# Optimization experiments

Measured on AMD Instinct MI355X. Metric: run time of the kernel, lower is better.

The kernel has to match this reference:

```python
import jax, jax.numpy as jnp
import numpy as np

S, B, E, H, AW = 4096, 2, 768, 12, 512  # seq, batch, embed, heads, attention_window


def _longformer_local_attn(query, Wq, bq, Wk, bk, Wv, bv):
    # query: [S, B, E] (seq-first, as in the torch module); returns [S, B, E]
    S_, B_, E_ = query.shape
    H_ = H
    D = E_ // H_
    W = AW // 2  # one-sided window (HF Longformer uses window//2 each side)
    x = query.transpose(1, 0, 2)  # [B, S, E]

    q = (x @ Wq + bq).reshape(B_, S_, H_, D) * (1.0 / jnp.sqrt(jnp.asarray(D, x.dtype)))
    k = (x @ Wk + bk).reshape(B_, S_, H_, D)
    v = (x @ Wv + bv).reshape(B_, S_, H_, D)

    nc = S_ // W  # number of query chunks of size W
    # pad keys/values by W on each side so every chunk sees a 3W key window
    kp = jnp.pad(k, ((0, 0), (W, W), (0, 0), (0, 0)))
    vp = jnp.pad(v, ((0, 0), (W, W), (0, 0), (0, 0)))
    # padded-coordinate indices of the 3W key window for each chunk: [nc, 3W]
    idx = jnp.arange(nc)[:, None] * W + jnp.arange(3 * W)[None, :]
    kc = kp[:, idx]  # [B, nc, 3W, H, D]
    vc = vp[:, idx]  # [B, nc, 3W, H, D]
    qc = q.reshape(B_, nc, W, H_, D)

    # banded scores: [B, H, nc, W, 3W]
    scores = jnp.einsum('bcqhd,bckhd->bhcqk', qc, kc)

    # mask: within-band (|rel| <= W) and inside the real sequence
    rel = (jnp.arange(3 * W) - W)[None, :] - jnp.arange(W)[:, None]  # [W, 3W]
    band = jnp.abs(rel) <= W
    abs_k = idx - W  # absolute key index, [nc, 3W]
    in_seq = (abs_k >= 0) & (abs_k < S_)
    mask = band[None, :, :] & in_seq[:, None, :]  # [nc, W, 3W]

    scores = jnp.where(mask[None, None], scores, -jnp.inf)
    attn = jax.nn.softmax(scores, axis=-1)
    out = jnp.einsum('bhcqk,bckhd->bcqhd', attn, vc).reshape(B_, S_, E_)
    return out.transpose(1, 0, 2)  # back to [S, B, E]


def setup_inputs() -> dict:
    key = jax.random.key(0)
    ks = jax.random.split(key, 4)
    scale = 0.02
    return {
        'query': jax.random.normal(ks[0], (S, B, E), jnp.float32),
        'Wq': jax.random.normal(ks[1], (E, E), jnp.float32) * scale,
        'bq': jnp.zeros((E,), jnp.float32),
        'Wk': jax.random.normal(ks[2], (E, E), jnp.float32) * scale,
        'bk': jnp.zeros((E,), jnp.float32),
        'Wv': jax.random.normal(ks[3], (E, E), jnp.float32) * scale,
        'bv': jnp.zeros((E,), jnp.float32),
    }


def reference(query, Wq, bq, Wk, bk, Wv, bv):
    # dropout is identity in eval mode; no global tokens (global mask defaults to zeros)
    return _longformer_local_attn(query, Wq, bq, Wk, bk, Wv, bv)
```

## Files before the change

### kernel.cpp

```cpp
#include <hip/hip_runtime.h>

#define S_ 4096
#define B_ 2
#define E_ 768
#define H_ 12
#define D_ 64

typedef __attribute__((ext_vector_type(8))) short short8;
typedef __attribute__((ext_vector_type(4))) float f32x4;
typedef unsigned short u16;
typedef unsigned int u32;

__device__ __forceinline__ u16 f2bf(float f) {
  union { float f; u32 u; } v; v.f = f;
  u32 r = v.u + 0x7FFFu + ((v.u >> 16) & 1u);
  return (u16)(r >> 16);
}

__device__ __forceinline__ void gl_lds16(const void* g, void* l) {
  __builtin_amdgcn_global_load_lds((const __attribute__((address_space(1))) u32*)g,
                                   (__attribute__((address_space(3))) u32*)l, 16, 0, 0);
}

__global__ __launch_bounds__(192) void k_convert_x(const float* __restrict__ q,
                                                   u16* __restrict__ x) {
  int m = blockIdx.x;
  int e = threadIdx.x * 4;
  int b = m >> 12, s = m & 4095;
  const float4 v = *(const float4*)&q[((s << 1) + b) * 768 + e];
  ushort4 o;
  o.x = f2bf(v.x); o.y = f2bf(v.y); o.z = f2bf(v.z); o.w = f2bf(v.w);
  *(ushort4*)&x[m * 768 + e] = o;
}

__global__ __launch_bounds__(256) void k_transpose_w(const float* __restrict__ w0,
                                                     const float* __restrict__ w1,
                                                     const float* __restrict__ w2,
                                                     u16* __restrict__ wt) {
  __shared__ float tile[32][33];
  const float* w = blockIdx.z == 0 ? w0 : (blockIdx.z == 1 ? w1 : w2);
  int k0 = blockIdx.x * 32, n0 = blockIdx.y * 32;
  int tx = threadIdx.x & 31, ty = threadIdx.x >> 5;
#pragma unroll
  for (int i = 0; i < 4; i++)
    tile[ty + i * 8][tx] = w[(k0 + ty + i * 8) * 768 + n0 + tx];
  __syncthreads();
  u16* o = wt + blockIdx.z * 768 * 768;
#pragma unroll
  for (int i = 0; i < 4; i++)
    o[(n0 + ty + i * 8) * 768 + k0 + tx] = f2bf(tile[tx][ty + i * 8]);
}

__global__ __launch_bounds__(256) void k_gemm_qkv(
    const u16* __restrict__ x, const u16* __restrict__ wt,
    const float* __restrict__ bq, const float* __restrict__ bk,
    const float* __restrict__ bv,
    u16* __restrict__ qb, u16* __restrict__ kb, u16* __restrict__ vt) {
  __shared__ __align__(16) u16 As[128 * 32];
  __shared__ __align__(16) u16 Bs[128 * 32];
  const int tid = threadIdx.x;
  const int lane = tid & 63, wave = tid >> 6;
  const int m0 = blockIdx.x * 128, n0 = blockIdx.y * 128, z = blockIdx.z;
  const u16* wz = wt + z * 768 * 768;
  const int wr = wave >> 1, wc = wave & 1;
  const int l15 = lane & 15, lg = lane >> 4;

  f32x4 acc[4][4] = {};

  for (int kt = 0; kt < 768; kt += 32) {
#pragma unroll
    for (int c = 0; c < 2; c++) {
      int ci = c * 256 + tid;
      int row = ci >> 2, cp = ci & 3;
      gl_lds16(&x[(size_t)(m0 + row) * 768 + kt + cp * 8],
               &As[(c * 256 + wave * 64) * 8]);
      gl_lds16(&wz[(size_t)(n0 + row) * 768 + kt + cp * 8],
               &Bs[(c * 256 + wave * 64) * 8]);
    }
    __syncthreads();
    short8 a[4], b[4];
#pragma unroll
    for (int mf = 0; mf < 4; mf++)
      a[mf] = *(const short8*)&As[(wr * 64 + mf * 16 + l15) * 32 + lg * 8];
#pragma unroll
    for (int nf = 0; nf < 4; nf++)
      b[nf] = *(const short8*)&Bs[(wc * 64 + nf * 16 + l15) * 32 + lg * 8];
#pragma unroll
    for (int mf = 0; mf < 4; mf++)
#pragma unroll
      for (int nf = 0; nf < 4; nf++)
        acc[mf][nf] = __builtin_amdgcn_mfma_f32_16x16x32_bf16(a[mf], b[nf], acc[mf][nf], 0, 0, 0);
    __syncthreads();
  }

  const float* bias_p = (z == 0) ? bq : (z == 1 ? bk : bv);
#pragma unroll
  for (int nf = 0; nf < 4; nf++) {
    int n = n0 + wc * 64 + nf * 16 + l15;
    float bias = bias_p[n];
#pragma unroll
    for (int mf = 0; mf < 4; mf++) {
      int mrow = m0 + wr * 64 + mf * 16 + lg * 4;
      if (z == 2) {
        int h = n >> 6, d = n & 63;
        int bb = mrow >> 12, s = mrow & 4095;
        ushort4 pk;
        pk.x = f2bf(acc[mf][nf][0] + bias);
        pk.y = f2bf(acc[mf][nf][1] + bias);
        pk.z = f2bf(acc[mf][nf][2] + bias);
        pk.w = f2bf(acc[mf][nf][3] + bias);
        *(ushort4*)&vt[(size_t)(((bb * 12 + h) * 64 + d) << 12) + s] = pk;
      } else {
        u16* t = (z == 0) ? qb : kb;
        float sc = (z == 0) ? 0.125f : 1.0f;
#pragma unroll
        for (int r = 0; r < 4; r++)
          t[(size_t)(mrow + r) * 768 + n] = f2bf((acc[mf][nf][r] + bias) * sc);
      }
    }
  }
}

__global__ __launch_bounds__(256) void k_attn(const u16* __restrict__ qb,
                                              const u16* __restrict__ kb,
                                              const u16* __restrict__ vt,
                                              float* __restrict__ out) {
  __shared__ __align__(16) u16 Ks[2][64 * 64];
  __shared__ __align__(16) u16 Vs[2][64 * 64];
  __shared__ __align__(16) u16 pl[4][32 * 72];
  const int tid = threadIdx.x;
  const int lane = tid & 63, wave = tid >> 6;
  const int l15 = lane & 15, lg = lane >> 4;

  const int bid = blockIdx.x;
  const int xcd = bid & 7, i = bid >> 3;
  const int pair = xcd * 3 + (i >> 5);
  const int chunk = i & 31;
  const int b = pair / 12, h = pair % 12;
  const int s0 = chunk * 128;
  const int q0 = s0 + wave * 32;

  short8 qf[2][2];
#pragma unroll
  for (int mf = 0; mf < 2; mf++)
#pragma unroll
    for (int ks = 0; ks < 2; ks++)
      qf[mf][ks] = *(const short8*)&qb[(size_t)((b << 12) + q0 + mf * 16 + l15) * 768 +
                                       h * 64 + ks * 32 + lg * 8];

  f32x4 o[2][4] = {};
  float lsum[2][4] = {};

  int t0 = s0 - 256; if (t0 < 0) t0 = 0;
  int t1 = s0 + 320; if (t1 > 4032) t1 = 4032;

  auto stage = [&](int buf, int kb0) {
#pragma unroll
    for (int c = 0; c < 2; c++) {
      int ci = c * 256 + tid;
      int row = ci >> 3, cc = ci & 7;
      int sc = cc ^ (row & 7);
      gl_lds16(&kb[(size_t)((b << 12) + kb0 + row) * 768 + h * 64 + sc * 8],
               &Ks[buf][(c * 256 + wave * 64) * 8]);
      gl_lds16(&vt[((size_t)((b * 12 + h) * 64 + row) << 12) + kb0 + sc * 8],
               &Vs[buf][(c * 256 + wave * 64) * 8]);
    }
  };

  stage(0, t0);
  int buf = 0;
  for (int kb0 = t0; kb0 <= t1; kb0 += 64) {
    if (kb0 + 64 <= t1) stage(buf ^ 1, kb0 + 64);
    __syncthreads();
    const bool act = (kb0 + 63 >= q0 - 256) && (kb0 <= q0 + 31 + 256);
    if (act) {
      f32x4 sf[2][4] = {};
#pragma unroll
      for (int ks = 0; ks < 2; ks++) {
        short8 bkf[4];
#pragma unroll
        for (int nf = 0; nf < 4; nf++) {
          int row = nf * 16 + l15;
          bkf[nf] = *(const short8*)&Ks[buf][row * 64 + (((ks * 4 + lg) ^ (row & 7)) * 8)];
        }
#pragma unroll
        for (int mf = 0; mf < 2; mf++)
#pragma unroll
          for (int nf = 0; nf < 4; nf++)
            sf[mf][nf] = __builtin_amdgcn_mfma_f32_16x16x32_bf16(qf[mf][ks], bkf[nf], sf[mf][nf], 0, 0, 0);
      }
      if (kb0 < q0 - 192 || kb0 > q0 + 192) {
#pragma unroll
        for (int mf = 0; mf < 2; mf++)
#pragma unroll
          for (int nf = 0; nf < 4; nf++) {
            int kj = kb0 + nf * 16 + l15;
#pragma unroll
            for (int r = 0; r < 4; r++) {
              int qi = q0 + mf * 16 + lg * 4 + r;
              if ((unsigned)(kj - qi + 256) > 512u) sf[mf][nf][r] = -3e38f;
            }
          }
      }
      u16* plw = pl[wave];
#pragma unroll
      for (int mf = 0; mf < 2; mf++)
#pragma unroll
        for (int nf = 0; nf < 4; nf++)
#pragma unroll
          for (int r = 0; r < 4; r++) {
            float p = __expf(sf[mf][nf][r]);
            lsum[mf][r] += p;
            plw[(mf * 16 + lg * 4 + r) * 72 + nf * 16 + l15] = f2bf(p);
          }
      short8 pa[2][2];
#pragma unroll
      for (int mf = 0; mf < 2; mf++)
#pragma unroll
        for (int ks = 0; ks < 2; ks++)
          pa[mf][ks] = *(const short8*)&plw[(mf * 16 + l15) * 72 + ks * 32 + lg * 8];
#pragma unroll
      for (int ks = 0; ks < 2; ks++) {
        short8 bvf[4];
#pragma unroll
        for (int df = 0; df < 4; df++) {
          int row = df * 16 + l15;
          bvf[df] = *(const short8*)&Vs[buf][row * 64 + (((ks * 4 + lg) ^ (row & 7)) * 8)];
        }
#pragma unroll
        for (int mf = 0; mf < 2; mf++)
#pragma unroll
          for (int df = 0; df < 4; df++)
            o[mf][df] = __builtin_amdgcn_mfma_f32_16x16x32_bf16(pa[mf][ks], bvf[df], o[mf][df], 0, 0, 0);
      }
    }
    __syncthreads();
    buf ^= 1;
  }

#pragma unroll
  for (int mf = 0; mf < 2; mf++)
#pragma unroll
    for (int r = 0; r < 4; r++) {
      float l = lsum[mf][r];
      l += __shfl_xor(l, 1); l += __shfl_xor(l, 2);
      l += __shfl_xor(l, 4); l += __shfl_xor(l, 8);
      lsum[mf][r] = l;
    }

#pragma unroll
  for (int mf = 0; mf < 2; mf++)
#pragma unroll
    for (int df = 0; df < 4; df++)
#pragma unroll
      for (int r = 0; r < 4; r++) {
        int s = q0 + mf * 16 + lg * 4 + r;
        out[(size_t)(s * 2 + b) * 768 + h * 64 + df * 16 + l15] =
            o[mf][df][r] / lsum[mf][r];
      }
}

extern "C" void kernel_launch(void* const* d_in, const int* in_sizes, int n_in,
                              void* d_out, int out_size, void* d_ws, size_t ws_size,
                              hipStream_t stream) {
  const float* query = (const float*)d_in[0];
  const float* Wq = (const float*)d_in[1];
  const float* bq = (const float*)d_in[2];
  const float* Wk = (const float*)d_in[3];
  const float* bk = (const float*)d_in[4];
  const float* Wv = (const float*)d_in[5];
  const float* bv = (const float*)d_in[6];
  float* out = (float*)d_out;

  char* ws = (char*)d_ws;
  size_t off = 0;
  auto alloc = [&](size_t bytes) {
    void* p = ws + off;
    off = (off + bytes + 255) & ~(size_t)255;
    return p;
  };
  u16* x  = (u16*)alloc((size_t)8192 * 768 * 2);
  u16* wt = (u16*)alloc((size_t)3 * 768 * 768 * 2);
  u16* qb = (u16*)alloc((size_t)8192 * 768 * 2);
  u16* kb = (u16*)alloc((size_t)8192 * 768 * 2);
  u16* vt = (u16*)alloc((size_t)8192 * 768 * 2);

  hipLaunchKernelGGL(k_convert_x, dim3(8192), dim3(192), 0, stream, query, x);
  hipLaunchKernelGGL(k_transpose_w, dim3(24, 24, 3), dim3(256), 0, stream, Wq, Wk, Wv, wt);
  hipLaunchKernelGGL(k_gemm_qkv, dim3(64, 6, 3), dim3(256), 0, stream,
                     x, wt, bq, bk, bv, qb, kb, vt);
  hipLaunchKernelGGL(k_attn, dim3(768), dim3(256), 0, stream, qb, kb, vt, out);
}
```

Before: 184.1 us.

## Double-buffer QKV GEMM, remap blocks per XCD, stage epilogue through LDS

Splits the QKV GEMM's LDS staging into two buffers so the next K-slice's global-to-LDS load is issued while the current slice runs MFMAs, which removes one barrier per iteration. The grid becomes 1D and is remapped so each XCD works on a contiguous group of row tiles, sharing the activation rows in its L2. The epilogue writes results into LDS first and then stores 16-byte vectors, replacing scattered 2-byte stores for Q/K and 8-byte stores for the transposed V. The cost is more shared memory per block, which may reduce occupancy.

```diff
diff --git a/kernel.cpp b/kernel.cpp
--- a/kernel.cpp
+++ b/kernel.cpp
@@ -56,35 +56,44 @@
     const float* __restrict__ bq, const float* __restrict__ bk,
     const float* __restrict__ bv,
     u16* __restrict__ qb, u16* __restrict__ kb, u16* __restrict__ vt) {
-  __shared__ __align__(16) u16 As[128 * 32];
-  __shared__ __align__(16) u16 Bs[128 * 32];
+  __shared__ __align__(16) u16 smem[18432];
   const int tid = threadIdx.x;
   const int lane = tid & 63, wave = tid >> 6;
-  const int m0 = blockIdx.x * 128, n0 = blockIdx.y * 128, z = blockIdx.z;
+  const int bid = blockIdx.x;
+  const int xcd = bid & 7, idx = bid >> 3;
+  const int m_l = idx / 18, rem = idx % 18;
+  const int n_i = rem / 3, z = rem % 3;
+  const int m0 = (xcd * 8 + m_l) * 128, n0 = n_i * 128;
   const u16* wz = wt + z * 768 * 768;
   const int wr = wave >> 1, wc = wave & 1;
   const int l15 = lane & 15, lg = lane >> 4;
 
   f32x4 acc[4][4] = {};
 
-  for (int kt = 0; kt < 768; kt += 32) {
+  auto stage = [&](int buf, int kt) {
 #pragma unroll
     for (int c = 0; c < 2; c++) {
       int ci = c * 256 + tid;
       int row = ci >> 2, cp = ci & 3;
       gl_lds16(&x[(size_t)(m0 + row) * 768 + kt + cp * 8],
-               &As[(c * 256 + wave * 64) * 8]);
+               &smem[buf * 4096 + (c * 256 + wave * 64) * 8]);
       gl_lds16(&wz[(size_t)(n0 + row) * 768 + kt + cp * 8],
-               &Bs[(c * 256 + wave * 64) * 8]);
-    }
-    __syncthreads();
+               &smem[8192 + buf * 4096 + (c * 256 + wave * 64) * 8]);
+    }
+  };
+
+  stage(0, 0);
+  __syncthreads();
+  for (int t = 0; t < 24; t++) {
+    const int buf = t & 1;
+    if (t < 23) stage(buf ^ 1, (t + 1) * 32);
     short8 a[4], b[4];
 #pragma unroll
     for (int mf = 0; mf < 4; mf++)
-      a[mf] = *(const short8*)&As[(wr * 64 + mf * 16 + l15) * 32 + lg * 8];
+      a[mf] = *(const short8*)&smem[buf * 4096 + (wr * 64 + mf * 16 + l15) * 32 + lg * 8];
 #pragma unroll
     for (int nf = 0; nf < 4; nf++)
-      b[nf] = *(const short8*)&Bs[(wc * 64 + nf * 16 + l15) * 32 + lg * 8];
+      b[nf] = *(const short8*)&smem[8192 + buf * 4096 + (wc * 64 + nf * 16 + l15) * 32 + lg * 8];
 #pragma unroll
     for (int mf = 0; mf < 4; mf++)
 #pragma unroll
@@ -93,30 +102,54 @@
     __syncthreads();
   }
 
+  u16* ep = &smem[wave * 4608];
   const float* bias_p = (z == 0) ? bq : (z == 1 ? bk : bv);
-#pragma unroll
-  for (int nf = 0; nf < 4; nf++) {
-    int n = n0 + wc * 64 + nf * 16 + l15;
-    float bias = bias_p[n];
-#pragma unroll
-    for (int mf = 0; mf < 4; mf++) {
-      int mrow = m0 + wr * 64 + mf * 16 + lg * 4;
-      if (z == 2) {
-        int h = n >> 6, d = n & 63;
-        int bb = mrow >> 12, s = mrow & 4095;
+  const int r8 = lane >> 3, cn = lane & 7;
+  if (z < 2) {
+    const float sc = (z == 0) ? 0.125f : 1.0f;
+#pragma unroll
+    for (int nf = 0; nf < 4; nf++) {
+      int n = n0 + wc * 64 + nf * 16 + l15;
+      float bias = bias_p[n];
+#pragma unroll
+      for (int mf = 0; mf < 4; mf++)
+#pragma unroll
+        for (int r = 0; r < 4; r++)
+          ep[(mf * 16 + lg * 4 + r) * 72 + nf * 16 + l15] =
+              f2bf((acc[mf][nf][r] + bias) * sc);
+    }
+    __syncthreads();
+    u16* t = (z == 0) ? qb : kb;
+#pragma unroll
+    for (int i = 0; i < 8; i++) {
+      int rl = i * 8 + r8;
+      short8 v = *(const short8*)&ep[rl * 72 + cn * 8];
+      *(short8*)&t[(size_t)(m0 + wr * 64 + rl) * 768 + n0 + wc * 64 + cn * 8] = v;
+    }
+  } else {
+#pragma unroll
+    for (int nf = 0; nf < 4; nf++) {
+      int n = n0 + wc * 64 + nf * 16 + l15;
+      float bias = bias_p[n];
+#pragma unroll
+      for (int mf = 0; mf < 4; mf++) {
         ushort4 pk;
         pk.x = f2bf(acc[mf][nf][0] + bias);
         pk.y = f2bf(acc[mf][nf][1] + bias);
         pk.z = f2bf(acc[mf][nf][2] + bias);
         pk.w = f2bf(acc[mf][nf][3] + bias);
-        *(ushort4*)&vt[(size_t)(((bb * 12 + h) * 64 + d) << 12) + s] = pk;
-      } else {
-        u16* t = (z == 0) ? qb : kb;
-        float sc = (z == 0) ? 0.125f : 1.0f;
-#pragma unroll
-        for (int r = 0; r < 4; r++)
-          t[(size_t)(mrow + r) * 768 + n] = f2bf((acc[mf][nf][r] + bias) * sc);
-      }
+        *(ushort4*)&ep[(nf * 16 + l15) * 72 + mf * 16 + lg * 4] = pk;
+      }
+    }
+    __syncthreads();
+    const int bb = m0 >> 12, srow = m0 & 4095;
+#pragma unroll
+    for (int i = 0; i < 8; i++) {
+      int nl = i * 8 + r8;
+      int n = n0 + wc * 64 + nl;
+      int h = n >> 6, d = n & 63;
+      short8 v = *(const short8*)&ep[nl * 72 + cn * 8];
+      *(short8*)&vt[(((size_t)(bb * 12 + h) * 64 + d) << 12) + srow + wr * 64 + cn * 8] = v;
     }
   }
 }
@@ -287,7 +320,7 @@
 
   hipLaunchKernelGGL(k_convert_x, dim3(8192), dim3(192), 0, stream, query, x);
   hipLaunchKernelGGL(k_transpose_w, dim3(24, 24, 3), dim3(256), 0, stream, Wq, Wk, Wv, wt);
-  hipLaunchKernelGGL(k_gemm_qkv, dim3(64, 6, 3), dim3(256), 0, stream,
+  hipLaunchKernelGGL(k_gemm_qkv, dim3(1152), dim3(256), 0, stream,
                      x, wt, bq, bk, bv, qb, kb, vt);
   hipLaunchKernelGGL(k_attn, dim3(768), dim3(256), 0, stream, qb, kb, vt, out);
 }
```

Result: faster. 173.0 us (-6.0%).
